# Performance work log

Measured on AMD Instinct MI355X. Metric: run time of the kernel, lower is better.

The kernel has to match this reference:

```python
import jax, jax.numpy as jnp
import numpy as np

PS = 7        # patch (window) size
DIM = 192     # channels
HEADS = 8
HID = 768     # mlp hidden = 4*dim
B = 8
HH = 112
WW = 112
EPS = 1e-5


def _rel_pos_index(ps):
    coords = np.stack(np.meshgrid(np.arange(ps), np.arange(ps), indexing='ij'))
    cf = coords.reshape(2, -1)
    rel = (cf[:, :, None] - cf[:, None, :]).transpose(1, 2, 0).astype(np.int64)
    rel[:, :, 0] += ps - 1
    rel[:, :, 1] += ps - 1
    rel[:, :, 0] *= 2 * ps - 1
    return rel.sum(-1)  # (N, N)

REL_IDX = jnp.asarray(_rel_pos_index(PS))  # (49, 49) int


def layer_norm(x, g, b):
    m = jnp.mean(x, axis=-1, keepdims=True)
    v = jnp.var(x, axis=-1, keepdims=True)
    return (x - m) * jax.lax.rsqrt(v + EPS) * g + b


def setup_inputs() -> dict:
    key = jax.random.key(0)
    ks = jax.random.split(key, 8)
    s = 0.02
    return {
        'x': jax.random.normal(ks[0], (B, HH * WW, DIM), jnp.float32),
        'norm1_g': jnp.ones((DIM,), jnp.float32),
        'norm1_b': jnp.zeros((DIM,), jnp.float32),
        'q_w': jax.random.normal(ks[1], (DIM, DIM), jnp.float32) * s,
        'q_b': jnp.zeros((DIM,), jnp.float32),
        'kv_w': jax.random.normal(ks[2], (2 * DIM, DIM), jnp.float32) * s,
        'kv_b': jnp.zeros((2 * DIM,), jnp.float32),
        'rpe_table': jax.random.normal(ks[3], ((2 * PS - 1) ** 2, HEADS), jnp.float32) * s,
        'proj_w': jax.random.normal(ks[4], (DIM, DIM), jnp.float32) * s,
        'proj_b': jnp.zeros((DIM,), jnp.float32),
        'norm2_g': jnp.ones((DIM,), jnp.float32),
        'norm2_b': jnp.zeros((DIM,), jnp.float32),
        'fc1_w': jax.random.normal(ks[5], (HID, DIM), jnp.float32) * s,
        'fc1_b': jnp.zeros((HID,), jnp.float32),
        'dw_w': jax.random.normal(ks[6], (HID, 1, 3, 3), jnp.float32) * s,
        'dw_b': jnp.zeros((HID,), jnp.float32),
        'fc2_w': jax.random.normal(ks[7], (DIM, HID), jnp.float32) * s,
        'fc2_b': jnp.zeros((DIM,), jnp.float32),
        'H': HH,
        'W': WW,
    }


def reference(x, norm1_g, norm1_b, q_w, q_b, kv_w, kv_b, rpe_table,
              proj_w, proj_b, norm2_g, norm2_b, fc1_w, fc1_b, dw_w, dw_b,
              fc2_w, fc2_b, H, W):
    Bsz, L, C = x.shape
    N = PS * PS
    hd = C // HEADS
    scale = hd ** -0.5
    nh, nw = H // PS, W // PS  # H, W chosen divisible by PS -> no padding

    shortcut = x
    xn = layer_norm(x, norm1_g, norm1_b)
    xi = xn.reshape(Bsz, H, W, C)
    # partition into non-overlapping PS x PS windows: (B*nP, N, C)
    p = xi.reshape(Bsz, nh, PS, nw, PS, C).transpose(0, 1, 3, 2, 4, 5).reshape(-1, N, C)

    # IPSA window attention (memory == x, T = 1)
    q = (p @ q_w.T + q_b).reshape(-1, N, HEADS, hd).transpose(0, 2, 1, 3) * scale
    kv = (p @ kv_w.T + kv_b).reshape(-1, N, 2, HEADS, hd).transpose(2, 0, 3, 1, 4)
    k, v = kv[0], kv[1]  # (B_, heads, N, hd)
    attn = jnp.einsum('bhnd,bhmd->bhnm', q, k)
    bias = rpe_table[REL_IDX.reshape(-1)].reshape(N, N, HEADS).transpose(2, 0, 1)
    attn = jax.nn.softmax(attn + bias[None], axis=-1)
    out = jnp.einsum('bhnm,bhmd->bhnd', attn, v).transpose(0, 2, 1, 3).reshape(-1, N, C)
    out = out @ proj_w.T + proj_b
    # reverse window partition back to (B, L, C)
    out = out.reshape(Bsz, nh, nw, PS, PS, C).transpose(0, 1, 3, 2, 4, 5).reshape(Bsz, L, C)
    x = shortcut + out

    # MLP with depthwise conv
    y = layer_norm(x, norm2_g, norm2_b)
    y = y @ fc1_w.T + fc1_b  # (B, L, HID)
    yc = y.transpose(0, 2, 1).reshape(Bsz, HID, H, W)
    yc = jax.lax.conv_general_dilated(
        yc, dw_w, window_strides=(1, 1), padding=((1, 1), (1, 1)),
        dimension_numbers=('NCHW', 'OIHW', 'NCHW'), feature_group_count=HID,
    ) + dw_b[None, :, None, None]
    y = yc.reshape(Bsz, HID, L).transpose(0, 2, 1)
    y = jax.nn.gelu(y, approximate=False)
    y = y @ fc2_w.T + fc2_b
    return x + y
```

## Files before the change

kernel.cpp:

```cpp
#include <hip/hip_runtime.h>
#include <hip/hip_bf16.h>
#include <cmath>

#define C_DIM 192
#define HID 768

typedef __attribute__((ext_vector_type(8))) __bf16 bf16x8;
typedef __attribute__((ext_vector_type(4))) float f32x4;
typedef __attribute__((ext_vector_type(2))) float f32x2;
typedef __attribute__((ext_vector_type(8))) unsigned short u16x8;
typedef __attribute__((ext_vector_type(4))) unsigned int u32x4;

__device__ __forceinline__ void gload_lds16(const void* g, void* l) {
  __builtin_amdgcn_global_load_lds(
      (__attribute__((address_space(1))) void*)(const_cast<void*>(g)),
      (__attribute__((address_space(3))) void*)(l), 16, 0, 0);
}

__device__ __forceinline__ float bfu2f(ushort u) {
  return __uint_as_float((unsigned)u << 16);
}
__device__ __forceinline__ ushort f2bfu(float f) {
  __hip_bfloat16 h = __float2bfloat16(f);
  return *reinterpret_cast<ushort*>(&h);
}
__device__ __forceinline__ float fgelu(float x) {
  float z = x * (1.5957691216f + 0.071354816f * x * x);
  return x / (1.f + __expf(-z));
}

__global__ __launch_bounds__(256) void prep_kernel(
    const float* __restrict__ q_w, const float* __restrict__ q_b,
    const float* __restrict__ kv_w, const float* __restrict__ kv_b,
    const float* __restrict__ proj_w, const float* __restrict__ fc1_w,
    const float* __restrict__ fc2_w,
    __hip_bfloat16* __restrict__ wcat, float* __restrict__ bcat,
    __hip_bfloat16* __restrict__ projw, __hip_bfloat16* __restrict__ fc1w,
    __hip_bfloat16* __restrict__ fc2w)
{
  int idx = blockIdx.x * 256 + threadIdx.x;
  const float scale = 0.20412414523193154f;
  if (idx < 110592) {
    float v = (idx < 36864) ? q_w[idx] * scale : kv_w[idx - 36864];
    wcat[idx] = __float2bfloat16(v);
  }
  if (idx < 576) bcat[idx] = (idx < 192) ? q_b[idx] * scale : kv_b[idx - 192];
  if (idx < 36864) projw[idx] = __float2bfloat16(proj_w[idx]);
  if (idx < 147456) {
    fc1w[idx] = __float2bfloat16(fc1_w[idx]);
    fc2w[idx] = __float2bfloat16(fc2_w[idx]);
  }
}

__global__ __launch_bounds__(256) void ln_kernel(
    const float* __restrict__ x, const float* __restrict__ g,
    const float* __restrict__ b, __hip_bfloat16* __restrict__ out)
{
  int t = blockIdx.x * 4 + (threadIdx.x >> 6);
  int lane = threadIdx.x & 63;
  const float* xr = x + (size_t)t * C_DIM;
  float v0 = xr[lane], v1 = xr[lane + 64], v2 = xr[lane + 128];
  float s = v0 + v1 + v2;
  float sq = v0 * v0 + v1 * v1 + v2 * v2;
  #pragma unroll
  for (int off = 32; off > 0; off >>= 1) {
    s += __shfl_xor(s, off, 64);
    sq += __shfl_xor(sq, off, 64);
  }
  float mean = s * (1.0f / 192.0f);
  float var = sq * (1.0f / 192.0f) - mean * mean;
  float rstd = rsqrtf(var + 1e-5f);
  size_t o = (size_t)t * C_DIM;
  out[o + lane]       = __float2bfloat16((v0 - mean) * rstd * g[lane] + b[lane]);
  out[o + lane + 64]  = __float2bfloat16((v1 - mean) * rstd * g[lane + 64] + b[lane + 64]);
  out[o + lane + 128] = __float2bfloat16((v2 - mean) * rstd * g[lane + 128] + b[lane + 128]);
}

template <int EPI>
__global__ __launch_bounds__(512, 4) void gemmA_kernel(
    const ushort* __restrict__ X, int lda, const ushort* __restrict__ W,
    const float* __restrict__ bias, const float* __restrict__ addin,
    void* __restrict__ outp, int N)
{
  __shared__ __align__(16) ushort Al[128 * 192];
  __shared__ __align__(16) ushort Bl[64 * 192];
  const int tid = threadIdx.x;
  const int wv = tid >> 6;
  const int lane = tid & 63;
  const int quad = lane >> 4;
  const int m15 = lane & 15;
  const long mBase = (long)blockIdx.y * 128;
  const int NT = N >> 6;

  #pragma unroll
  for (int r = 0; r < 6; ++r) {
    int sI = tid + r * 512;
    int row = sI / 24;
    int cs = sI - row * 24;
    int gc = cs - (row % 24); if (gc < 0) gc += 24;
    gload_lds16(X + (mBase + row) * (long)lda + gc * 8, Al + sI * 8);
  }

  const int rA0 = wv * 16 + m15;
  const int rA0m = rA0 % 24;

  for (int nt = 0; nt < NT; ++nt) {
    __syncthreads();
    #pragma unroll
    for (int r = 0; r < 3; ++r) {
      int sI = tid + r * 512;
      int row = sI / 24;
      int cs = sI - row * 24;
      int gc = cs - (row % 24); if (gc < 0) gc += 24;
      gload_lds16(W + (long)(nt * 64 + row) * 192 + gc * 8, Bl + sI * 8);
    }
    __syncthreads();

    f32x4 acc[4];
    #pragma unroll
    for (int c = 0; c < 4; ++c) acc[c] = (f32x4){0.f, 0.f, 0.f, 0.f};

    #pragma unroll
    for (int ks = 0; ks < 6; ++ks) {
      const int l = ks * 4 + quad;
      int pa0 = l + rA0m; if (pa0 >= 24) pa0 -= 24;
      bf16x8 a0 = *(const bf16x8*)&Al[rA0 * 192 + pa0 * 8];
      #pragma unroll
      for (int ct = 0; ct < 4; ++ct) {
        const int rB = ct * 16 + m15;
        int pb = l + (rB % 24); if (pb >= 24) pb -= 24;
        bf16x8 b = *(const bf16x8*)&Bl[rB * 192 + pb * 8];
        acc[ct] = __builtin_amdgcn_mfma_f32_16x16x32_bf16(a0, b, acc[ct], 0, 0, 0);
      }
    }
    #pragma unroll
    for (int ct = 0; ct < 4; ++ct)
      #pragma unroll
      for (int i = 0; i < 4; ++i) {
        long row = mBase + wv * 16 + quad * 4 + i;
        int col = nt * 64 + ct * 16 + m15;
        float v = acc[ct][i] + bias[col];
        if (EPI == 1) {
          v += addin[row * N + col];
          ((float*)outp)[row * N + col] = v;
        } else {
          ((__hip_bfloat16*)outp)[row * N + col] = __float2bfloat16(v);
        }
      }
  }
}

__global__ __launch_bounds__(512, 4) void gemmA_ln_kernel(
    const ushort* __restrict__ X, int lda, const ushort* __restrict__ W,
    const float* __restrict__ bias, const float* __restrict__ addin,
    float* __restrict__ outp, const float* __restrict__ lng,
    const float* __restrict__ lnb, __hip_bfloat16* __restrict__ xnout)
{
  __shared__ __align__(16) ushort Al[128 * 192];
  __shared__ __align__(16) ushort Bl[64 * 192];
  const int tid = threadIdx.x;
  const int wv = tid >> 6;
  const int lane = tid & 63;
  const int quad = lane >> 4;
  const int m15 = lane & 15;
  const long mBase = (long)blockIdx.y * 128;

  #pragma unroll
  for (int r = 0; r < 6; ++r) {
    int sI = tid + r * 512;
    int row = sI / 24;
    int cs = sI - row * 24;
    int gc = cs - (row % 24); if (gc < 0) gc += 24;
    gload_lds16(X + (mBase + row) * (long)lda + gc * 8, Al + sI * 8);
  }

  const int rA0 = wv * 16 + m15;
  const int rA0m = rA0 % 24;

  f32x4 acc[3][4];
  #pragma unroll
  for (int n = 0; n < 3; ++n)
    #pragma unroll
    for (int c = 0; c < 4; ++c) acc[n][c] = (f32x4){0.f, 0.f, 0.f, 0.f};

  #pragma unroll
  for (int nt = 0; nt < 3; ++nt) {
    __syncthreads();
    #pragma unroll
    for (int r = 0; r < 3; ++r) {
      int sI = tid + r * 512;
      int row = sI / 24;
      int cs = sI - row * 24;
      int gc = cs - (row % 24); if (gc < 0) gc += 24;
      gload_lds16(W + (long)(nt * 64 + row) * 192 + gc * 8, Bl + sI * 8);
    }
    __syncthreads();
    #pragma unroll
    for (int ks = 0; ks < 6; ++ks) {
      const int l = ks * 4 + quad;
      int pa0 = l + rA0m; if (pa0 >= 24) pa0 -= 24;
      bf16x8 a0 = *(const bf16x8*)&Al[rA0 * 192 + pa0 * 8];
      #pragma unroll
      for (int ct = 0; ct < 4; ++ct) {
        const int rB = ct * 16 + m15;
        int pb = l + (rB % 24); if (pb >= 24) pb -= 24;
        bf16x8 b = *(const bf16x8*)&Bl[rB * 192 + pb * 8];
        acc[nt][ct] = __builtin_amdgcn_mfma_f32_16x16x32_bf16(a0, b, acc[nt][ct], 0, 0, 0);
      }
    }
  }

  float sum_[4], sq_[4];
  #pragma unroll
  for (int i = 0; i < 4; ++i) { sum_[i] = 0.f; sq_[i] = 0.f; }

  #pragma unroll
  for (int nt = 0; nt < 3; ++nt)
    #pragma unroll
    for (int ct = 0; ct < 4; ++ct) {
      int col = nt * 64 + ct * 16 + m15;
      float cb = bias[col];
      #pragma unroll
      for (int i = 0; i < 4; ++i) {
        long row = mBase + wv * 16 + quad * 4 + i;
        float v = acc[nt][ct][i] + cb + addin[row * 192 + col];
        outp[row * 192 + col] = v;
        acc[nt][ct][i] = v;
        sum_[i] += v;
        sq_[i] += v * v;
      }
    }

  float mean_[4], rstd_[4];
  #pragma unroll
  for (int i = 0; i < 4; ++i) {
    float s = sum_[i], q = sq_[i];
    #pragma unroll
    for (int m = 1; m < 16; m <<= 1) {
      s += __shfl_xor(s, m, 64);
      q += __shfl_xor(q, m, 64);
    }
    float mean = s * (1.0f / 192.0f);
    mean_[i] = mean;
    rstd_[i] = rsqrtf(q * (1.0f / 192.0f) - mean * mean + 1e-5f);
  }

  #pragma unroll
  for (int nt = 0; nt < 3; ++nt)
    #pragma unroll
    for (int ct = 0; ct < 4; ++ct) {
      int col = nt * 64 + ct * 16 + m15;
      float cg = lng[col], cbb = lnb[col];
      #pragma unroll
      for (int i = 0; i < 4; ++i) {
        long row = mBase + wv * 16 + quad * 4 + i;
        float v = (acc[nt][ct][i] - mean_[i]) * rstd_[i] * cg + cbb;
        xnout[row * 192 + col] = __float2bfloat16(v);
      }
    }
}

__global__ __launch_bounds__(512, 4) void gemmB_kernel(
    const ushort* __restrict__ X, const ushort* __restrict__ W,
    const float* __restrict__ bias, const float* __restrict__ addin,
    float* __restrict__ outp)
{
  __shared__ __align__(16) ushort Al[128 * 192];
  __shared__ __align__(16) ushort Bl[64 * 192];
  const int tid = threadIdx.x;
  const int wv = tid >> 6;
  const int lane = tid & 63;
  const int quad = lane >> 4;
  const int m15 = lane & 15;
  const long mBase = (long)blockIdx.y * 128;

  const int rA0 = wv * 16 + m15;
  const int rA0m = rA0 % 24;

  f32x4 acc[3][4];
  #pragma unroll
  for (int n = 0; n < 3; ++n)
    #pragma unroll
    for (int c = 0; c < 4; ++c) acc[n][c] = (f32x4){0.f, 0.f, 0.f, 0.f};

  for (int kc = 0; kc < 4; ++kc) {
    for (int nt = 0; nt < 3; ++nt) {
      __syncthreads();
      if (nt == 0) {
        #pragma unroll
        for (int r = 0; r < 6; ++r) {
          int sI = tid + r * 512;
          int row = sI / 24;
          int cs = sI - row * 24;
          int gc = cs - (row % 24); if (gc < 0) gc += 24;
          gload_lds16(X + (mBase + row) * 768l + kc * 192 + gc * 8, Al + sI * 8);
        }
      }
      #pragma unroll
      for (int r = 0; r < 3; ++r) {
        int sI = tid + r * 512;
        int row = sI / 24;
        int cs = sI - row * 24;
        int gc = cs - (row % 24); if (gc < 0) gc += 24;
        gload_lds16(W + (long)(nt * 64 + row) * 768 + kc * 192 + gc * 8, Bl + sI * 8);
      }
      __syncthreads();
      #pragma unroll
      for (int ks = 0; ks < 6; ++ks) {
        const int l = ks * 4 + quad;
        int pa0 = l + rA0m; if (pa0 >= 24) pa0 -= 24;
        bf16x8 a0 = *(const bf16x8*)&Al[rA0 * 192 + pa0 * 8];
        #pragma unroll
        for (int ct = 0; ct < 4; ++ct) {
          const int rB = ct * 16 + m15;
          int pb = l + (rB % 24); if (pb >= 24) pb -= 24;
          bf16x8 b = *(const bf16x8*)&Bl[rB * 192 + pb * 8];
          acc[nt][ct] = __builtin_amdgcn_mfma_f32_16x16x32_bf16(a0, b, acc[nt][ct], 0, 0, 0);
        }
      }
    }
  }
  #pragma unroll
  for (int nt = 0; nt < 3; ++nt)
    #pragma unroll
    for (int ct = 0; ct < 4; ++ct)
      #pragma unroll
      for (int i = 0; i < 4; ++i) {
        long row = mBase + wv * 16 + quad * 4 + i;
        int col = nt * 64 + ct * 16 + m15;
        float v = acc[nt][ct][i] + bias[col] + addin[row * 192 + col];
        outp[row * 192 + col] = v;
      }
}

__global__ __launch_bounds__(256, 3) void attn_kernel(
    const float* __restrict__ rpe, __hip_bfloat16* __restrict__ qkv)
{
  __shared__ __align__(16) char smem[51968];
  const int tid = threadIdx.x;
  const int lane = tid & 63;
  const int wv = tid >> 6;
  const int quad = lane >> 4;
  const int m15 = lane & 15;
  const int wh = blockIdx.x * 4 + wv;
  const int h = wh & 7;
  const int win = wh >> 3;
  const int b = win >> 8;
  const int wl = win & 255;
  const int whi = wl >> 4;
  const int wwi = wl & 15;
  ushort* qkv_u = (ushort*)qkv;
  char* Vb = smem + wv * 4096;
  char* Pb = smem + 16384 + wv * 8192;
  float* biasW = (float*)(smem + 49152 + wv * 704);

  const long rowbase = (long)b * 12544 + (long)(whi * 7) * 112 + wwi * 7;

  {
    int j = lane;
    int f = ((j >> 3) & 3) << 5;
    if (j < 49) {
      int py = j / 7, px = j - py * 7;
      long row = rowbase + py * 112 + px;
      const ushort* src = qkv_u + row * 576 + 384 + h * 24;
      #pragma unroll
      for (int c = 0; c < 3; ++c) {
        u16x8 val = *(const u16x8*)(src + c * 8);
        *(u16x8*)(Vb + ((j * 64 + c * 16) ^ f)) = val;
      }
    } else {
      u16x8 z = {};
      #pragma unroll
      for (int c = 0; c < 4; ++c)
        *(u16x8*)(Vb + ((j * 64 + c * 16) ^ f)) = z;
    }
  }
  for (int r = lane; r < 169; r += 64) biasW[r] = rpe[r * 8 + h];

  int bi[4];
  #pragma unroll
  for (int rt = 0; rt < 4; ++rt) {
    int r = rt * 16 + m15; if (r > 48) r = 48;
    bi[rt] = (r / 7) * 13 + (r % 7) + 84;
  }
  int bj4[4][4];
  #pragma unroll
  for (int jt = 0; jt < 4; ++jt)
    #pragma unroll
    for (int i = 0; i < 4; ++i) {
      int j = jt * 16 + quad * 4 + i; if (j > 48) j = 48;
      bj4[jt][i] = (j / 7) * 13 + (j % 7);
    }

  f32x4 sacc[4][4];
  #pragma unroll
  for (int jt = 0; jt < 4; ++jt)
    #pragma unroll
    for (int rt = 0; rt < 4; ++rt)
      #pragma unroll
      for (int i = 0; i < 4; ++i)
        sacc[jt][rt][i] = biasW[bi[rt] - bj4[jt][i]];

  bf16x8 kf[4], qf[4];
  const bf16x8 zf = {};
  #pragma unroll
  for (int jt = 0; jt < 4; ++jt) {
    int t = jt * 16 + m15; if (t > 48) t = 48;
    long row = rowbase + (t / 7) * 112 + (t % 7);
    kf[jt] = *(const bf16x8*)(qkv_u + row * 576 + 192 + h * 24 + quad * 8);
    if (quad == 3) kf[jt] = zf;
  }
  #pragma unroll
  for (int rt = 0; rt < 4; ++rt) {
    int t = rt * 16 + m15; if (t > 48) t = 48;
    long row = rowbase + (t / 7) * 112 + (t % 7);
    qf[rt] = *(const bf16x8*)(qkv_u + row * 576 + h * 24 + quad * 8);
  }
  #pragma unroll
  for (int jt = 0; jt < 4; ++jt)
    #pragma unroll
    for (int rt = 0; rt < 4; ++rt)
      sacc[jt][rt] = __builtin_amdgcn_mfma_f32_16x16x32_bf16(
          kf[jt], qf[rt], sacc[jt][rt], 0, 0, 0);

  #pragma unroll
  for (int rt = 0; rt < 4; ++rt) {
    if (quad != 0) sacc[3][rt][0] = -1e30f;
    sacc[3][rt][1] = -1e30f;
    sacc[3][rt][2] = -1e30f;
    sacc[3][rt][3] = -1e30f;
  }

  float inv[4];
  #pragma unroll
  for (int rt = 0; rt < 4; ++rt) {
    float mx = sacc[0][rt][0];
    #pragma unroll
    for (int jt = 0; jt < 4; ++jt)
      #pragma unroll
      for (int i = 0; i < 4; ++i)
        mx = fmaxf(mx, sacc[jt][rt][i]);
    mx = fmaxf(mx, __shfl_xor(mx, 16, 64));
    mx = fmaxf(mx, __shfl_xor(mx, 32, 64));
    float sum = 0.f;
    #pragma unroll
    for (int jt = 0; jt < 4; ++jt)
      #pragma unroll
      for (int i = 0; i < 4; ++i) {
        float p = __expf(sacc[jt][rt][i] - mx);
        sacc[jt][rt][i] = p;
        sum += p;
      }
    sum += __shfl_xor(sum, 16, 64);
    sum += __shfl_xor(sum, 32, 64);
    inv[rt] = 1.f / sum;
  }

  const int swzP = (m15 & 7) << 4;
  #pragma unroll
  for (int rt = 0; rt < 4; ++rt)
    #pragma unroll
    for (int jt = 0; jt < 4; ++jt)
      #pragma unroll
      for (int u = 0; u < 2; ++u) {
        unsigned pk;
        asm("v_cvt_pk_bf16_f32 %0, %1, %2"
            : "=v"(pk)
            : "v"(sacc[jt][rt][2 * u]), "v"(sacc[jt][rt][2 * u + 1]));
        int j0 = jt * 16 + quad * 4 + 2 * u;
        int lin = (rt * 16 + m15) * 128 + j0 * 2;
        *(unsigned*)(Pb + (lin ^ swzP)) = pk;
      }

  f32x4 oacc[4][2];
  #pragma unroll
  for (int mt = 0; mt < 4; ++mt)
    #pragma unroll
    for (int nt = 0; nt < 2; ++nt) oacc[mt][nt] = (f32x4){0.f, 0.f, 0.f, 0.f};

  #pragma unroll
  for (int kt = 0; kt < 2; ++kt) {
    bf16x8 pf[4];
    #pragma unroll
    for (int mt = 0; mt < 4; ++mt) {
      int lin = (mt * 16 + m15) * 128 + kt * 64 + quad * 16;
      pf[mt] = *(const bf16x8*)(Pb + (lin ^ swzP));
    }
    bf16x8 vf[2];
    #pragma unroll
    for (int nt = 0; nt < 2; ++nt) {
      u32x4 w;
      #pragma unroll
      for (int e2 = 0; e2 < 4; ++e2) {
        int j_lo = kt * 32 + quad * 8 + 2 * e2;
        int lin_lo = j_lo * 64 + (nt * 16 + m15) * 2;
        int lin_hi = lin_lo + 64;
        unsigned lo = *(const ushort*)(Vb + (lin_lo ^ (quad << 5)));
        unsigned hi = *(const ushort*)(Vb + (lin_hi ^ (quad << 5)));
        w[e2] = lo | (hi << 16);
      }
      vf[nt] = __builtin_bit_cast(bf16x8, w);
    }
    #pragma unroll
    for (int mt = 0; mt < 4; ++mt)
      #pragma unroll
      for (int nt = 0; nt < 2; ++nt)
        oacc[mt][nt] = __builtin_amdgcn_mfma_f32_16x16x32_bf16(
            pf[mt], vf[nt], oacc[mt][nt], 0, 0, 0);
  }

  #pragma unroll
  for (int mt = 0; mt < 4; ++mt)
    #pragma unroll
    for (int i = 0; i < 4; ++i) {
      float iv = __shfl(inv[mt], quad * 4 + i, 64);
      int r = mt * 16 + quad * 4 + i;
      if (r < 49) {
        long row = rowbase + (r / 7) * 112 + (r % 7);
        ushort* dst = qkv_u + row * 576 + h * 24;
        dst[m15] = f2bfu(oacc[mt][0][i] * iv);
        if (m15 < 8) dst[16 + m15] = f2bfu(oacc[mt][1][i] * iv);
      }
    }
}

__global__ __launch_bounds__(192) void dwconv_gelu_kernel(
    const ushort* __restrict__ y1, const float* __restrict__ w,
    const float* __restrict__ bias, ushort* __restrict__ y2)
{
  const int c = threadIdx.x * 4;
  const int w0 = blockIdx.y * 2;
  const int b = blockIdx.z;
  const int h0 = blockIdx.x * 28;

  float wt[9][4];
  #pragma unroll
  for (int k = 0; k < 9; ++k)
    #pragma unroll
    for (int j = 0; j < 4; ++j) wt[k][j] = w[(c + j) * 9 + k];
  float bs[4];
  #pragma unroll
  for (int j = 0; j < 4; ++j) bs[j] = bias[c + j];

  const bool okL = (w0 > 0), okR = (w0 + 2 < 112);
  ushort4 rb[6][4];

  auto loadrow = [&](int h, ushort4 dst[4]) {
    const ushort4 z = {0, 0, 0, 0};
    if (h < 0 || h >= 112) {
      dst[0] = z; dst[1] = z; dst[2] = z; dst[3] = z;
      return;
    }
    const ushort* p = y1 + (((size_t)(b * 112 + h)) * 112 + w0) * HID + c;
    dst[0] = okL ? *(const ushort4*)(p - HID) : z;
    dst[1] = *(const ushort4*)(p);
    dst[2] = *(const ushort4*)(p + HID);
    dst[3] = okR ? *(const ushort4*)(p + 2 * HID) : z;
  };

  loadrow(h0 - 1, rb[0]);
  loadrow(h0, rb[1]);

  for (int m = 0; m < 7; ++m) {
    const int hb = h0 + m * 4;
    loadrow(hb + 1, rb[2]);
    loadrow(hb + 2, rb[3]);
    loadrow(hb + 3, rb[4]);
    loadrow(hb + 4, rb[5]);
    #pragma unroll
    for (int o = 0; o < 4; ++o) {
      float acc0[4], acc1[4];
      #pragma unroll
      for (int j = 0; j < 4; ++j) { acc0[j] = bs[j]; acc1[j] = bs[j]; }
      #pragma unroll
      for (int dy = 0; dy < 3; ++dy) {
        float col[4][4];
        #pragma unroll
        for (int x = 0; x < 4; ++x) {
          ushort4 u = rb[o + dy][x];
          col[x][0] = bfu2f(u.x); col[x][1] = bfu2f(u.y);
          col[x][2] = bfu2f(u.z); col[x][3] = bfu2f(u.w);
        }
        #pragma unroll
        for (int dx = 0; dx < 3; ++dx)
          #pragma unroll
          for (int j = 0; j < 4; ++j) {
            acc0[j] += wt[dy * 3 + dx][j] * col[dx][j];
            acc1[j] += wt[dy * 3 + dx][j] * col[dx + 1][j];
          }
      }
      ushort* outp = y2 + (((size_t)(b * 112 + hb + o)) * 112 + w0) * HID + c;
      ushort4 o0, o1;
      o0.x = f2bfu(fgelu(acc0[0])); o0.y = f2bfu(fgelu(acc0[1]));
      o0.z = f2bfu(fgelu(acc0[2])); o0.w = f2bfu(fgelu(acc0[3]));
      o1.x = f2bfu(fgelu(acc1[0])); o1.y = f2bfu(fgelu(acc1[1]));
      o1.z = f2bfu(fgelu(acc1[2])); o1.w = f2bfu(fgelu(acc1[3]));
      *(ushort4*)(outp) = o0;
      *(ushort4*)(outp + HID) = o1;
    }
    #pragma unroll
    for (int x = 0; x < 4; ++x) {
      rb[0][x] = rb[4][x];
      rb[1][x] = rb[5][x];
    }
  }
}

extern "C" void kernel_launch(void* const* d_in, const int* in_sizes, int n_in,
                              void* d_out, int out_size, void* d_ws, size_t ws_size,
                              hipStream_t stream) {
  const float* x      = (const float*)d_in[0];
  const float* n1g    = (const float*)d_in[1];
  const float* n1b    = (const float*)d_in[2];
  const float* q_w    = (const float*)d_in[3];
  const float* q_b    = (const float*)d_in[4];
  const float* kv_w   = (const float*)d_in[5];
  const float* kv_b   = (const float*)d_in[6];
  const float* rpe    = (const float*)d_in[7];
  const float* proj_w = (const float*)d_in[8];
  const float* proj_b = (const float*)d_in[9];
  const float* n2g    = (const float*)d_in[10];
  const float* n2b    = (const float*)d_in[11];
  const float* fc1_w  = (const float*)d_in[12];
  const float* fc1_b  = (const float*)d_in[13];
  const float* dw_w   = (const float*)d_in[14];
  const float* dw_b   = (const float*)d_in[15];
  const float* fc2_w  = (const float*)d_in[16];
  const float* fc2_b  = (const float*)d_in[17];
  float* out = (float*)d_out;

  char* ws = (char*)d_ws;
  __hip_bfloat16* wcat  = (__hip_bfloat16*)(ws);
  __hip_bfloat16* projw = (__hip_bfloat16*)(ws + 221184);
  __hip_bfloat16* fc1w  = (__hip_bfloat16*)(ws + 294912);
  __hip_bfloat16* fc2w  = (__hip_bfloat16*)(ws + 589824);
  float* bcat           = (float*)(ws + 884736);
  const size_t WOFF = 1u << 20;

  int CB = 8;
  while (CB > 1 && WOFF + (size_t)CB * 12544 * 3456 > ws_size) CB >>= 1;
  const size_t Mc = (size_t)CB * 12544;
  char* Abuf = ws + WOFF;
  char* Bbuf = Abuf + Mc * 384;
  char* Cbuf = Bbuf + Mc * 1536;
  __hip_bfloat16* xn  = (__hip_bfloat16*)Abuf;
  __hip_bfloat16* qkv = (__hip_bfloat16*)Bbuf;
  __hip_bfloat16* y2  = (__hip_bfloat16*)Bbuf;
  __hip_bfloat16* y1  = (__hip_bfloat16*)Cbuf;

  prep_kernel<<<576, 256, 0, stream>>>(q_w, q_b, kv_w, kv_b, proj_w, fc1_w,
                                       fc2_w, wcat, bcat, projw, fc1w, fc2w);

  const int nChunks = 8 / CB;
  const int mt = CB * 98;
  for (int cchunk = 0; cchunk < nChunks; ++cchunk) {
    const size_t toff = (size_t)cchunk * Mc;
    const float* xc = x + toff * C_DIM;
    float* oc = out + toff * C_DIM;

    ln_kernel<<<(int)(Mc / 4), 256, 0, stream>>>(xc, n1g, n1b, xn);
    gemmA_kernel<0><<<dim3(1, mt), 512, 0, stream>>>(
        (const ushort*)xn, 192, (const ushort*)wcat, bcat, nullptr, qkv, 576);
    attn_kernel<<<CB * 512, 256, 0, stream>>>(rpe, qkv);
    gemmA_ln_kernel<<<dim3(1, mt), 512, 0, stream>>>(
        (const ushort*)qkv, 576, (const ushort*)projw, proj_b, xc, oc,
        n2g, n2b, xn);
    gemmA_kernel<0><<<dim3(1, mt), 512, 0, stream>>>(
        (const ushort*)xn, 192, (const ushort*)fc1w, fc1_b, nullptr, y1, 768);
    dwconv_gelu_kernel<<<dim3(4, 56, CB), 192, 0, stream>>>(
        (const ushort*)y1, dw_w, dw_b, (ushort*)y2);
    gemmB_kernel<<<dim3(1, mt), 512, 0, stream>>>(
        (const ushort*)y2, (const ushort*)fc2w, fc2_b, oc, oc);
  }
}
```

Measured before the change: 587.2 us.

## Restructure dwconv-GELU with packed f32x2 math, row prefetch ring, more blocks

The depthwise conv plus GELU kernel now gives each block 16 rows instead of 28, and the grid grows from 4 to 7 blocks along H. Rows are kept in a fully unrolled 10-slot register ring, so the next four rows load while the current four are computed. The arithmetic uses packed f32x2 FMAs, unpacks bf16 with shift and mask, and converts to bf16 with v_cvt_pk_bf16_f32. The goal is more latency hiding and parallelism plus fewer VALU instructions, at the cost of more register pressure and extra halo rows reloaded at block edges.

```diff
diff --git a/kernel.cpp b/kernel.cpp
--- a/kernel.cpp
+++ b/kernel.cpp
@@ -531,77 +531,82 @@
   const int c = threadIdx.x * 4;
   const int w0 = blockIdx.y * 2;
   const int b = blockIdx.z;
-  const int h0 = blockIdx.x * 28;
-
-  float wt[9][4];
-  #pragma unroll
-  for (int k = 0; k < 9; ++k)
-    #pragma unroll
-    for (int j = 0; j < 4; ++j) wt[k][j] = w[(c + j) * 9 + k];
-  float bs[4];
-  #pragma unroll
-  for (int j = 0; j < 4; ++j) bs[j] = bias[c + j];
+  const int h0 = blockIdx.x * 16;
+
+  f32x2 wt2[9][2];
+  #pragma unroll
+  for (int k = 0; k < 9; ++k) {
+    wt2[k][0] = (f32x2){w[(c + 0) * 9 + k], w[(c + 1) * 9 + k]};
+    wt2[k][1] = (f32x2){w[(c + 2) * 9 + k], w[(c + 3) * 9 + k]};
+  }
+  f32x2 bs2[2] = {(f32x2){bias[c], bias[c + 1]},
+                  (f32x2){bias[c + 2], bias[c + 3]}};
 
   const bool okL = (w0 > 0), okR = (w0 + 2 < 112);
-  ushort4 rb[6][4];
-
-  auto loadrow = [&](int h, ushort4 dst[4]) {
-    const ushort4 z = {0, 0, 0, 0};
+  uint2 rb[10][4];
+
+  auto loadrow = [&](int h, uint2 dst[4]) {
+    const uint2 z = {0u, 0u};
     if (h < 0 || h >= 112) {
       dst[0] = z; dst[1] = z; dst[2] = z; dst[3] = z;
       return;
     }
     const ushort* p = y1 + (((size_t)(b * 112 + h)) * 112 + w0) * HID + c;
-    dst[0] = okL ? *(const ushort4*)(p - HID) : z;
-    dst[1] = *(const ushort4*)(p);
-    dst[2] = *(const ushort4*)(p + HID);
-    dst[3] = okR ? *(const ushort4*)(p + 2 * HID) : z;
+    dst[0] = okL ? *(const uint2*)(p - HID) : z;
+    dst[1] = *(const uint2*)(p);
+    dst[2] = *(const uint2*)(p + HID);
+    dst[3] = okR ? *(const uint2*)(p + 2 * HID) : z;
   };
 
-  loadrow(h0 - 1, rb[0]);
-  loadrow(h0, rb[1]);
-
-  for (int m = 0; m < 7; ++m) {
-    const int hb = h0 + m * 4;
-    loadrow(hb + 1, rb[2]);
-    loadrow(hb + 2, rb[3]);
-    loadrow(hb + 3, rb[4]);
-    loadrow(hb + 4, rb[5]);
+  #pragma unroll
+  for (int s = 0; s < 6; ++s) loadrow(h0 - 1 + s, rb[s]);
+
+  #pragma unroll
+  for (int m = 0; m < 4; ++m) {
+    if (m < 3) {
+      #pragma unroll
+      for (int k = 0; k < 4; ++k)
+        loadrow(h0 + 4 * m + 5 + k, rb[(4 * m + 6 + k) % 10]);
+    }
     #pragma unroll
     for (int o = 0; o < 4; ++o) {
-      float acc0[4], acc1[4];
-      #pragma unroll
-      for (int j = 0; j < 4; ++j) { acc0[j] = bs[j]; acc1[j] = bs[j]; }
+      f32x2 a0[2], a1[2];
+      a0[0] = bs2[0]; a0[1] = bs2[1];
+      a1[0] = bs2[0]; a1[1] = bs2[1];
       #pragma unroll
       for (int dy = 0; dy < 3; ++dy) {
-        float col[4][4];
+        const int s = (4 * m + o + dy) % 10;
+        f32x2 col[4][2];
         #pragma unroll
         for (int x = 0; x < 4; ++x) {
-          ushort4 u = rb[o + dy][x];
-          col[x][0] = bfu2f(u.x); col[x][1] = bfu2f(u.y);
-          col[x][2] = bfu2f(u.z); col[x][3] = bfu2f(u.w);
+          unsigned lo = rb[s][x].x, hi = rb[s][x].y;
+          col[x][0] = (f32x2){__uint_as_float(lo << 16),
+                              __uint_as_float(lo & 0xffff0000u)};
+          col[x][1] = (f32x2){__uint_as_float(hi << 16),
+                              __uint_as_float(hi & 0xffff0000u)};
         }
         #pragma unroll
         for (int dx = 0; dx < 3; ++dx)
           #pragma unroll
-          for (int j = 0; j < 4; ++j) {
-            acc0[j] += wt[dy * 3 + dx][j] * col[dx][j];
-            acc1[j] += wt[dy * 3 + dx][j] * col[dx + 1][j];
+          for (int p = 0; p < 2; ++p) {
+            a0[p] += wt2[dy * 3 + dx][p] * col[dx][p];
+            a1[p] += wt2[dy * 3 + dx][p] * col[dx + 1][p];
           }
       }
-      ushort* outp = y2 + (((size_t)(b * 112 + hb + o)) * 112 + w0) * HID + c;
-      ushort4 o0, o1;
-      o0.x = f2bfu(fgelu(acc0[0])); o0.y = f2bfu(fgelu(acc0[1]));
-      o0.z = f2bfu(fgelu(acc0[2])); o0.w = f2bfu(fgelu(acc0[3]));
-      o1.x = f2bfu(fgelu(acc1[0])); o1.y = f2bfu(fgelu(acc1[1]));
-      o1.z = f2bfu(fgelu(acc1[2])); o1.w = f2bfu(fgelu(acc1[3]));
-      *(ushort4*)(outp) = o0;
-      *(ushort4*)(outp + HID) = o1;
-    }
-    #pragma unroll
-    for (int x = 0; x < 4; ++x) {
-      rb[0][x] = rb[4][x];
-      rb[1][x] = rb[5][x];
+      ushort* outp = y2 + (((size_t)(b * 112 + h0 + 4 * m + o)) * 112 + w0) * HID + c;
+      unsigned p0, p1, p2, p3;
+      {
+        float g0 = fgelu(a0[0][0]), g1 = fgelu(a0[0][1]);
+        float g2 = fgelu(a0[1][0]), g3 = fgelu(a0[1][1]);
+        asm("v_cvt_pk_bf16_f32 %0, %1, %2" : "=v"(p0) : "v"(g0), "v"(g1));
+        asm("v_cvt_pk_bf16_f32 %0, %1, %2" : "=v"(p1) : "v"(g2), "v"(g3));
+        float h0f = fgelu(a1[0][0]), h1f = fgelu(a1[0][1]);
+        float h2f = fgelu(a1[1][0]), h3f = fgelu(a1[1][1]);
+        asm("v_cvt_pk_bf16_f32 %0, %1, %2" : "=v"(p2) : "v"(h0f), "v"(h1f));
+        asm("v_cvt_pk_bf16_f32 %0, %1, %2" : "=v"(p3) : "v"(h2f), "v"(h3f));
+      }
+      *(uint2*)(outp) = (uint2){p0, p1};
+      *(uint2*)(outp + HID) = (uint2){p2, p3};
     }
   }
 }
@@ -667,7 +672,7 @@
         n2g, n2b, xn);
     gemmA_kernel<0><<<dim3(1, mt), 512, 0, stream>>>(
         (const ushort*)xn, 192, (const ushort*)fc1w, fc1_b, nullptr, y1, 768);
-    dwconv_gelu_kernel<<<dim3(4, 56, CB), 192, 0, stream>>>(
+    dwconv_gelu_kernel<<<dim3(7, 56, CB), 192, 0, stream>>>(
         (const ushort*)y1, dw_w, dw_b, (ushort*)y2);
     gemmB_kernel<<<dim3(1, mt), 512, 0, stream>>>(
         (const ushort*)y2, (const ushort*)fc2w, fc2_b, oc, oc);
```

Measured after the change: 586.9 us. Within noise of the previous version (-0.0%).

## Restructure depthwise conv to 2 channels per thread with rolling row buffer

Applied to the files above, without the earlier changes.

Rewrites the depthwise conv + GELU kernel so each thread handles 2 channels instead of 4, with 384-thread blocks and 16-row strips over more blocks. It switches from a 4-row batched load to a rolling 4-row register window with packed f32x2 math, and uses a hardware packed bf16 conversion instruction. The aim is lower register pressure, higher occupancy and more parallelism in this memory-bound stage. The cost is narrower 4-byte loads and stores and more halo-row reloads per output.

```diff
diff --git a/kernel.cpp b/kernel.cpp
--- a/kernel.cpp
+++ b/kernel.cpp
@@ -524,85 +524,77 @@
     }
 }
 
-__global__ __launch_bounds__(192) void dwconv_gelu_kernel(
+__global__ __launch_bounds__(384, 8) void dwconv_gelu_kernel(
     const ushort* __restrict__ y1, const float* __restrict__ w,
     const float* __restrict__ bias, ushort* __restrict__ y2)
 {
-  const int c = threadIdx.x * 4;
+  const int c = threadIdx.x * 2;
   const int w0 = blockIdx.y * 2;
   const int b = blockIdx.z;
-  const int h0 = blockIdx.x * 28;
-
-  float wt[9][4];
+  const int h0 = blockIdx.x * 16;
+
+  f32x2 wt[9];
   #pragma unroll
   for (int k = 0; k < 9; ++k)
-    #pragma unroll
-    for (int j = 0; j < 4; ++j) wt[k][j] = w[(c + j) * 9 + k];
-  float bs[4];
-  #pragma unroll
-  for (int j = 0; j < 4; ++j) bs[j] = bias[c + j];
+    wt[k] = (f32x2){w[(c + 0) * 9 + k], w[(c + 1) * 9 + k]};
+  const f32x2 bs = (f32x2){bias[c], bias[c + 1]};
 
   const bool okL = (w0 > 0), okR = (w0 + 2 < 112);
-  ushort4 rb[6][4];
-
-  auto loadrow = [&](int h, ushort4 dst[4]) {
-    const ushort4 z = {0, 0, 0, 0};
+
+  uint rA[4], rB[4], rC[4], rD[4];
+
+  auto loadrow = [&](int h, uint dst[4]) {
     if (h < 0 || h >= 112) {
-      dst[0] = z; dst[1] = z; dst[2] = z; dst[3] = z;
+      dst[0] = 0u; dst[1] = 0u; dst[2] = 0u; dst[3] = 0u;
       return;
     }
     const ushort* p = y1 + (((size_t)(b * 112 + h)) * 112 + w0) * HID + c;
-    dst[0] = okL ? *(const ushort4*)(p - HID) : z;
-    dst[1] = *(const ushort4*)(p);
-    dst[2] = *(const ushort4*)(p + HID);
-    dst[3] = okR ? *(const ushort4*)(p + 2 * HID) : z;
+    dst[0] = okL ? *(const uint*)(p - HID) : 0u;
+    dst[1] = *(const uint*)(p);
+    dst[2] = *(const uint*)(p + HID);
+    dst[3] = okR ? *(const uint*)(p + 2 * HID) : 0u;
   };
 
-  loadrow(h0 - 1, rb[0]);
-  loadrow(h0, rb[1]);
-
-  for (int m = 0; m < 7; ++m) {
-    const int hb = h0 + m * 4;
-    loadrow(hb + 1, rb[2]);
-    loadrow(hb + 2, rb[3]);
-    loadrow(hb + 3, rb[4]);
-    loadrow(hb + 4, rb[5]);
-    #pragma unroll
-    for (int o = 0; o < 4; ++o) {
-      float acc0[4], acc1[4];
-      #pragma unroll
-      for (int j = 0; j < 4; ++j) { acc0[j] = bs[j]; acc1[j] = bs[j]; }
-      #pragma unroll
-      for (int dy = 0; dy < 3; ++dy) {
-        float col[4][4];
-        #pragma unroll
-        for (int x = 0; x < 4; ++x) {
-          ushort4 u = rb[o + dy][x];
-          col[x][0] = bfu2f(u.x); col[x][1] = bfu2f(u.y);
-          col[x][2] = bfu2f(u.z); col[x][3] = bfu2f(u.w);
-        }
-        #pragma unroll
-        for (int dx = 0; dx < 3; ++dx)
-          #pragma unroll
-          for (int j = 0; j < 4; ++j) {
-            acc0[j] += wt[dy * 3 + dx][j] * col[dx][j];
-            acc1[j] += wt[dy * 3 + dx][j] * col[dx + 1][j];
-          }
-      }
-      ushort* outp = y2 + (((size_t)(b * 112 + hb + o)) * 112 + w0) * HID + c;
-      ushort4 o0, o1;
-      o0.x = f2bfu(fgelu(acc0[0])); o0.y = f2bfu(fgelu(acc0[1]));
-      o0.z = f2bfu(fgelu(acc0[2])); o0.w = f2bfu(fgelu(acc0[3]));
-      o1.x = f2bfu(fgelu(acc1[0])); o1.y = f2bfu(fgelu(acc1[1]));
-      o1.z = f2bfu(fgelu(acc1[2])); o1.w = f2bfu(fgelu(acc1[3]));
-      *(ushort4*)(outp) = o0;
-      *(ushort4*)(outp + HID) = o1;
-    }
-    #pragma unroll
-    for (int x = 0; x < 4; ++x) {
-      rb[0][x] = rb[4][x];
-      rb[1][x] = rb[5][x];
-    }
+  loadrow(h0 - 1, rA);
+  loadrow(h0,     rB);
+  loadrow(h0 + 1, rC);
+  loadrow(h0 + 2, rD);
+
+  auto accum = [&](const uint r[4], int dy, f32x2& a0, f32x2& a1) {
+    f32x2 col[4];
+    #pragma unroll
+    for (int x = 0; x < 4; ++x)
+      col[x] = (f32x2){__uint_as_float(r[x] << 16),
+                       __uint_as_float(r[x] & 0xffff0000u)};
+    #pragma unroll
+    for (int dx = 0; dx < 3; ++dx) {
+      a0 += wt[dy * 3 + dx] * col[dx];
+      a1 += wt[dy * 3 + dx] * col[dx + 1];
+    }
+  };
+
+  #pragma unroll 4
+  for (int hh = 0; hh < 16; ++hh) {
+    const int h = h0 + hh;
+    f32x2 a0 = bs, a1 = bs;
+    accum(rA, 0, a0, a1);
+    accum(rB, 1, a0, a1);
+    accum(rC, 2, a0, a1);
+
+    ushort* outp = y2 + (((size_t)(b * 112 + h)) * 112 + w0) * HID + c;
+    unsigned q0, q1;
+    {
+      float g0 = fgelu(a0[0]), g1 = fgelu(a0[1]);
+      float g2 = fgelu(a1[0]), g3 = fgelu(a1[1]);
+      asm("v_cvt_pk_bf16_f32 %0, %1, %2" : "=v"(q0) : "v"(g0), "v"(g1));
+      asm("v_cvt_pk_bf16_f32 %0, %1, %2" : "=v"(q1) : "v"(g2), "v"(g3));
+    }
+    *(uint*)(outp) = q0;
+    *(uint*)(outp + HID) = q1;
+
+    #pragma unroll
+    for (int x = 0; x < 4; ++x) { rA[x] = rB[x]; rB[x] = rC[x]; rC[x] = rD[x]; }
+    loadrow(h + 3, rD);
   }
 }
 
@@ -667,7 +659,7 @@
         n2g, n2b, xn);
     gemmA_kernel<0><<<dim3(1, mt), 512, 0, stream>>>(
         (const ushort*)xn, 192, (const ushort*)fc1w, fc1_b, nullptr, y1, 768);
-    dwconv_gelu_kernel<<<dim3(4, 56, CB), 192, 0, stream>>>(
+    dwconv_gelu_kernel<<<dim3(7, 56, CB), 384, 0, stream>>>(
         (const ushort*)y1, dw_w, dw_b, (ushort*)y2);
     gemmB_kernel<<<dim3(1, mt), 512, 0, stream>>>(
         (const ushort*)y2, (const ushort*)fc2w, fc2_b, oc, oc);
```

Measured after the change: 585.4 us. About the same (-0.3%).
